# Kernel tuning notes

Hardware: AMD Instinct MI355X
Metric: run time of the kernel (lower is better)

Reference implementation:

```python
import jax, jax.numpy as jnp
import numpy as np
import math

HIDDEN = 8
HEADS = 2
HEAD_DIM = HIDDEN // HEADS  # 4
MAX_SEQ = 102
B, S = 4096, 102


def _rotary_cache(seq_len, head_dim):
    # Matches _create_rotary_embeddings: dim = head_dim//2, inv_freq over arange(0, dim, 2)
    pos = jnp.arange(seq_len, dtype=jnp.float32)
    dim = head_dim // 2
    inv_freq = 1.0 / (10000.0 ** (jnp.arange(0, dim, 2, dtype=jnp.float32) / dim))
    sinusoid = pos[:, None] * inv_freq[None, :]           # [seq, dim//2] -> [102, 1]
    return jnp.stack([jnp.sin(sinusoid), jnp.cos(sinusoid)], axis=0)  # [2, seq, 1]


def _apply_rotary(x, cos, sin):
    # x: [B, H, S, hd]; cos/sin: [2, S, 1] (faithful to the source's buggy unpack,
    # which broadcasts the stacked sin/cos pair across the H==2 head dim)
    x2 = jnp.stack([-x[..., 1::2], x[..., ::2]], axis=-1).reshape(x.shape)
    return x * cos + x2 * sin


def setup_inputs() -> dict:
    key = jax.random.key(0)
    kq, kk, kv, k1, k2, k3, k4 = jax.random.split(key, 7)
    scale = 1.0 / math.sqrt(HIDDEN)
    return {
        "query": jax.random.normal(kq, (B, S, HIDDEN), dtype=jnp.float32),
        "key": jax.random.normal(kk, (B, S, HIDDEN), dtype=jnp.float32),
        "value": jax.random.normal(kv, (B, S, HIDDEN), dtype=jnp.float32),
        "wq": jax.random.normal(k1, (HIDDEN, HIDDEN), dtype=jnp.float32) * scale,
        "wk": jax.random.normal(k2, (HIDDEN, HIDDEN), dtype=jnp.float32) * scale,
        "wv": jax.random.normal(k3, (HIDDEN, HIDDEN), dtype=jnp.float32) * scale,
        "wo": jax.random.normal(k4, (HIDDEN, HIDDEN), dtype=jnp.float32) * scale,
    }


def reference(query, key, value, wq, wk, wv, wo):
    b, sq, _ = query.shape
    sk = key.shape[1]
    # nn.Linear (no bias): y = x @ W^T
    q = query @ wq.T
    k = key @ wk.T
    v = value @ wv.T
    # b n (h d) -> b h n d
    def split_heads(t, s):
        return t.reshape(b, s, HEADS, HEAD_DIM).transpose(0, 2, 1, 3)
    q = split_heads(q, sq)
    k = split_heads(k, sk)
    v = split_heads(v, sk)
    cache = _rotary_cache(MAX_SEQ, HEAD_DIM)
    sin_t = cache[:, :sq]  # [2, sq, 1] (named 'sin' in source, holds stacked sin/cos)
    cos_t = cache[:, :sk]  # [2, sk, 1]
    q = _apply_rotary(q, cos_t, sin_t)
    k = _apply_rotary(k, cos_t, sin_t)
    scale = 1.0 / math.sqrt(HEAD_DIM)
    # chunk_size = min(sk, 1024) = sk -> single chunk == full softmax attention
    scores = jnp.einsum('bhqd,bhkd->bhqk', q, k) * scale  # [B, H, Sq, Sk]
    attn = jax.nn.softmax(scores, axis=-1)
    out = jnp.einsum('bhqk,bhkd->bhqd', attn, v)
    # b h n d -> b n (h d)
    out = out.transpose(0, 2, 1, 3).reshape(b, sq, HIDDEN)
    return out @ wo.T
```

## Files before the change

### kernel.cpp

```cpp
#include <hip/hip_runtime.h>

#define NB 4096
#define SS 102
#define QSCALE 0.72134752044448170368f

typedef float v2f __attribute__((ext_vector_type(2)));
typedef __fp16 h2 __attribute__((ext_vector_type(2)));
typedef __fp16 h8 __attribute__((ext_vector_type(8)));

__global__ __launch_bounds__(256) void mha_fused_kernel(
    const float* __restrict__ query, const float* __restrict__ key,
    const float* __restrict__ value, const float* __restrict__ wq,
    const float* __restrict__ wk, const float* __restrict__ wvp,
    const float* __restrict__ wo, float* __restrict__ out)
{
    __shared__ __align__(16) unsigned char lds[17264];
    float*  RAW  = (float*)lds;
    float*  QF   = (float*)(lds + 9792);
    float*  ROTT = (float*)(lds + 13120);
    __fp16* KV   = (__fp16*)(lds + 13936);
    float*  COMB = (float*)lds;
    float*  PART = (float*)(lds + 3264);

    const int t = threadIdx.x;
    const int b = blockIdx.x;

    float4 rq, rk, rv;
    if (t < 204) {
        const float4* q4 = (const float4*)(query + (size_t)b * 816);
        const float4* k4 = (const float4*)(key   + (size_t)b * 816);
        const float4* v4 = (const float4*)(value + (size_t)b * 816);
        rq = q4[t]; rk = k4[t]; rv = v4[t];
    }

    if (t < SS) {
        const float ang = (float)t;
        ROTT[2 * t]     = sinf(ang);
        ROTT[2 * t + 1] = cosf(ang);
    }
    if (t >= 208 && t < 212) {
        const int z = t - 208;
        *(float4*)(QF + (((z >> 1) * 104) + SS + (z & 1)) * 4) =
            (float4){0.f, 0.f, 0.f, 0.f};
    }

    if (t < 204) {
        float4* R4 = (float4*)RAW;
        R4[t]       = rq;
        R4[204 + t] = rk;
        R4[408 + t] = rv;
    }
    __syncthreads();

    {
        const int wvu  = __builtin_amdgcn_readfirstlane(t >> 6);
        const int lane = t & 63;
        if (wvu < 3) {
            const float* W = (wvu == 0) ? wq : (wvu == 1) ? wk : wvp;
            for (int r = lane; r < SS; r += 64) {
                const float4 a = *(const float4*)(RAW + (wvu * SS + r) * 8);
                const float4 c = *(const float4*)(RAW + (wvu * SS + r) * 8 + 4);
                float x[8];
#pragma unroll
                for (int ch = 0; ch < 8; ++ch) {
                    x[ch] = a.x * W[ch * 8 + 0] + a.y * W[ch * 8 + 1]
                          + a.z * W[ch * 8 + 2] + a.w * W[ch * 8 + 3]
                          + c.x * W[ch * 8 + 4] + c.y * W[ch * 8 + 5]
                          + c.z * W[ch * 8 + 6] + c.w * W[ch * 8 + 7];
                }
                if (wvu == 2) {
#pragma unroll
                    for (int h = 0; h < 2; ++h) {
                        __fp16* rec = KV + (h * 104 + r) * 8;
                        *(h2*)(rec + 4) = __builtin_amdgcn_cvt_pkrtz(x[4*h+0], x[4*h+1]);
                        *(h2*)(rec + 6) = __builtin_amdgcn_cvt_pkrtz(x[4*h+2], x[4*h+3]);
                    }
                } else {
                    const float2 sc = *(const float2*)(ROTT + 2 * r);
#pragma unroll
                    for (int h = 0; h < 2; ++h) {
                        float w = (h == 0) ? sc.x : sc.y;
                        if (wvu == 0) w *= QSCALE;
                        const float y0 = (x[4*h+0] - x[4*h+1]) * w;
                        const float y1 = (x[4*h+1] + x[4*h+0]) * w;
                        const float y2 = (x[4*h+2] - x[4*h+3]) * w;
                        const float y3 = (x[4*h+3] + x[4*h+2]) * w;
                        if (wvu == 0) {
                            *(float4*)(QF + (h * 104 + r) * 4) =
                                (float4){y0, y1, y2, y3};
                        } else {
                            __fp16* rec = KV + (h * 104 + r) * 8;
                            *(h2*)(rec)     = __builtin_amdgcn_cvt_pkrtz(y0, y1);
                            *(h2*)(rec + 2) = __builtin_amdgcn_cvt_pkrtz(y2, y3);
                        }
                    }
                }
            }
        }
    }
    __syncthreads();

    {
        const int wv   = t >> 6, lane = t & 63;
        const int h    = wv >> 1, kh = wv & 1;
        const bool act = lane < 52;
        v2f acc0 = {0.f, 0.f}, acc1 = {0.f, 0.f},
            acc2 = {0.f, 0.f}, acc3 = {0.f, 0.f}, L = {0.f, 0.f};
        if (act) {
            const float4 qa = *(const float4*)(QF + (h * 104 + 2 * lane) * 4);
            const float4 qc = *(const float4*)(QF + (h * 104 + 2 * lane + 1) * 4);
            const v2f q0 = {qa.x, qc.x}, q1 = {qa.y, qc.y},
                      q2 = {qa.z, qc.z}, q3 = {qa.w, qc.w};
            const __fp16* KVh = KV + (h * 104 + kh * 51) * 8;
            for (int j = 0; j < 51; ++j) {
                const h8 rec = *(const h8*)(KVh + j * 8);
                const float k0 = (float)rec[0], k1 = (float)rec[1];
                const float k2 = (float)rec[2], k3 = (float)rec[3];
                const float v0 = (float)rec[4], v1 = (float)rec[5];
                const float v2 = (float)rec[6], v3 = (float)rec[7];
                v2f s = q0 * k0 + q1 * k1 + q2 * k2 + q3 * k3;
                v2f p;
                p.x = __builtin_amdgcn_exp2f(s.x);
                p.y = __builtin_amdgcn_exp2f(s.y);
                L += p;
                acc0 += p * v0; acc1 += p * v1;
                acc2 += p * v2; acc3 += p * v3;
            }
            if (kh == 1) {
                float* P = PART + (h * 52 + lane) * 10;
                *(v2f*)(P + 0) = acc0; *(v2f*)(P + 2) = acc1;
                *(v2f*)(P + 4) = acc2; *(v2f*)(P + 6) = acc3;
                *(v2f*)(P + 8) = L;
            }
        }
        __syncthreads();
        if (act && kh == 0) {
            const float* P = PART + (h * 52 + lane) * 10;
            acc0 += *(const v2f*)(P + 0); acc1 += *(const v2f*)(P + 2);
            acc2 += *(const v2f*)(P + 4); acc3 += *(const v2f*)(P + 6);
            L    += *(const v2f*)(P + 8);
            const float a0[2] = {acc0.x, acc0.y}, a1[2] = {acc1.x, acc1.y};
            const float a2[2] = {acc2.x, acc2.y}, a3[2] = {acc3.x, acc3.y};
            const float ll[2] = {L.x, L.y};
#pragma unroll
            for (int j = 0; j < 2; ++j) {
                const int row = 2 * lane + j;
                if (row < SS) {
                    const float inv = 1.f / ll[j];
                    *(float4*)(COMB + row * 8 + h * 4) =
                        (float4){a0[j] * inv, a1[j] * inv, a2[j] * inv, a3[j] * inv};
                }
            }
        }
    }
    __syncthreads();

    if (t < SS) {
        const float4 a = *(const float4*)(COMB + t * 8);
        const float4 c = *(const float4*)(COMB + t * 8 + 4);
        float x[8];
#pragma unroll
        for (int ch = 0; ch < 8; ++ch) {
            x[ch] = a.x * wo[ch * 8 + 0] + a.y * wo[ch * 8 + 1]
                  + a.z * wo[ch * 8 + 2] + a.w * wo[ch * 8 + 3]
                  + c.x * wo[ch * 8 + 4] + c.y * wo[ch * 8 + 5]
                  + c.z * wo[ch * 8 + 6] + c.w * wo[ch * 8 + 7];
        }
        float* o = out + (size_t)b * 816 + t * 8;
        *(float4*)(o)     = (float4){x[0], x[1], x[2], x[3]};
        *(float4*)(o + 4) = (float4){x[4], x[5], x[6], x[7]};
    }
}

extern "C" void kernel_launch(void* const* d_in, const int* in_sizes, int n_in,
                              void* d_out, int out_size, void* d_ws, size_t ws_size,
                              hipStream_t stream) {
    const float* query = (const float*)d_in[0];
    const float* key   = (const float*)d_in[1];
    const float* value = (const float*)d_in[2];
    const float* wq    = (const float*)d_in[3];
    const float* wk    = (const float*)d_in[4];
    const float* wv    = (const float*)d_in[5];
    const float* wo    = (const float*)d_in[6];
    float* out = (float*)d_out;
    mha_fused_kernel<<<NB, 256, 0, stream>>>(query, key, value, wq, wk, wv, wo, out);
}
```

Measured before the change: 122.7 us.

## Map one batch element per wavefront with fp16 staging and fdot2 scores

Each wavefront now handles a whole batch element, so each 256-thread block covers four elements in private LDS slices and all __syncthreads barriers go away. Raw inputs and Q are staged in fp16, and attention scores use packed fdot2 on half pairs. Each lane now covers four query rows over all 102 keys, which removes the split-key partial combine. sin/cos come from fast intrinsics in registers instead of an LDS table. The costs are lower precision (inputs and Q rounded to fp16, plus approximate sin/cos at angles up to 101) and more registers per lane.

After: 121.4 us. About the same (-1.0%).

```diff
diff --git a/kernel.cpp b/kernel.cpp
--- a/kernel.cpp
+++ b/kernel.cpp
@@ -1,174 +1,162 @@
 #include <hip/hip_runtime.h>
 
-#define NB 4096
 #define SS 102
 #define QSCALE 0.72134752044448170368f
 
-typedef float v2f __attribute__((ext_vector_type(2)));
 typedef __fp16 h2 __attribute__((ext_vector_type(2)));
+typedef __fp16 h4 __attribute__((ext_vector_type(4)));
 typedef __fp16 h8 __attribute__((ext_vector_type(8)));
 
-__global__ __launch_bounds__(256) void mha_fused_kernel(
+__device__ __forceinline__ void store4h(__fp16* p, float a, float b,
+                                        float c, float d) {
+    h2 lo = __builtin_amdgcn_cvt_pkrtz(a, b);
+    h2 hi = __builtin_amdgcn_cvt_pkrtz(c, d);
+    *(h4*)p = __builtin_shufflevector(lo, hi, 0, 1, 2, 3);
+}
+
+__global__ __launch_bounds__(256, 4) void mha_fused_kernel(
     const float* __restrict__ query, const float* __restrict__ key,
     const float* __restrict__ value, const float* __restrict__ wq,
     const float* __restrict__ wk, const float* __restrict__ wvp,
     const float* __restrict__ wo, float* __restrict__ out)
 {
-    __shared__ __align__(16) unsigned char lds[17264];
-    float*  RAW  = (float*)lds;
-    float*  QF   = (float*)(lds + 9792);
-    float*  ROTT = (float*)(lds + 13120);
-    __fp16* KV   = (__fp16*)(lds + 13936);
-    float*  COMB = (float*)lds;
-    float*  PART = (float*)(lds + 3264);
+    __shared__ __align__(16) unsigned char lds[4 * 9792];
+    const int t = threadIdx.x;
+    const int w = t >> 6, lane = t & 63;
+    unsigned char* base = lds + w * 9792;
+    __fp16* RAWH = (__fp16*)base;
+    __fp16* QH   = (__fp16*)(base + 4896);
+    __fp16* KV   = (__fp16*)(base + 6528);
+    float*  COMB = (float*)base;
 
-    const int t = threadIdx.x;
-    const int b = blockIdx.x;
+    const size_t b = (size_t)blockIdx.x * 4 + w;
 
-    float4 rq, rk, rv;
-    if (t < 204) {
-        const float4* q4 = (const float4*)(query + (size_t)b * 816);
-        const float4* k4 = (const float4*)(key   + (size_t)b * 816);
-        const float4* v4 = (const float4*)(value + (size_t)b * 816);
-        rq = q4[t]; rk = k4[t]; rv = v4[t];
+    const float4* q4 = (const float4*)(query + b * 816);
+    const float4* k4 = (const float4*)(key   + b * 816);
+    const float4* v4 = (const float4*)(value + b * 816);
+    float4 rq[4], rk[4], rv[4];
+#pragma unroll
+    for (int c = 0; c < 4; ++c) {
+        const int i = lane + 64 * c;
+        if (i < 204) { rq[c] = q4[i]; rk[c] = k4[i]; rv[c] = v4[i]; }
+    }
+#pragma unroll
+    for (int c = 0; c < 4; ++c) {
+        const int i = lane + 64 * c;
+        if (i < 204) {
+            store4h(RAWH + i * 4,        rq[c].x, rq[c].y, rq[c].z, rq[c].w);
+            store4h(RAWH + 816 + i * 4,  rk[c].x, rk[c].y, rk[c].z, rk[c].w);
+            store4h(RAWH + 1632 + i * 4, rv[c].x, rv[c].y, rv[c].z, rv[c].w);
+        }
     }
 
-    if (t < SS) {
-        const float ang = (float)t;
-        ROTT[2 * t]     = sinf(ang);
-        ROTT[2 * t + 1] = cosf(ang);
+    float snv[2], csv[2];
+#pragma unroll
+    for (int c = 0; c < 2; ++c) {
+        const int r = lane + 64 * c;
+        snv[c] = __sinf((float)r);
+        csv[c] = __cosf((float)r);
     }
-    if (t >= 208 && t < 212) {
-        const int z = t - 208;
-        *(float4*)(QF + (((z >> 1) * 104) + SS + (z & 1)) * 4) =
-            (float4){0.f, 0.f, 0.f, 0.f};
-    }
-
-    if (t < 204) {
-        float4* R4 = (float4*)RAW;
-        R4[t]       = rq;
-        R4[204 + t] = rk;
-        R4[408 + t] = rv;
-    }
-    __syncthreads();
-
-    {
-        const int wvu  = __builtin_amdgcn_readfirstlane(t >> 6);
-        const int lane = t & 63;
-        if (wvu < 3) {
-            const float* W = (wvu == 0) ? wq : (wvu == 1) ? wk : wvp;
-            for (int r = lane; r < SS; r += 64) {
-                const float4 a = *(const float4*)(RAW + (wvu * SS + r) * 8);
-                const float4 c = *(const float4*)(RAW + (wvu * SS + r) * 8 + 4);
+#pragma unroll
+    for (int T = 0; T < 3; ++T) {
+        const float* W = (T == 0) ? wq : (T == 1) ? wk : wvp;
+#pragma unroll
+        for (int c = 0; c < 2; ++c) {
+            const int r = lane + 64 * c;
+            if (r < SS) {
+                const h8 raw = *(const h8*)(RAWH + T * 816 + r * 8);
                 float x[8];
 #pragma unroll
                 for (int ch = 0; ch < 8; ++ch) {
-                    x[ch] = a.x * W[ch * 8 + 0] + a.y * W[ch * 8 + 1]
-                          + a.z * W[ch * 8 + 2] + a.w * W[ch * 8 + 3]
-                          + c.x * W[ch * 8 + 4] + c.y * W[ch * 8 + 5]
-                          + c.z * W[ch * 8 + 6] + c.w * W[ch * 8 + 7];
+                    float acc = 0.f;
+#pragma unroll
+                    for (int j = 0; j < 8; ++j)
+                        acc += (float)raw[j] * W[ch * 8 + j];
+                    x[ch] = acc;
                 }
-                if (wvu == 2) {
+                if (T == 2) {
+                    store4h(KV + (0 * SS + r) * 8 + 4, x[0], x[1], x[2], x[3]);
+                    store4h(KV + (1 * SS + r) * 8 + 4, x[4], x[5], x[6], x[7]);
+                } else {
 #pragma unroll
                     for (int h = 0; h < 2; ++h) {
-                        __fp16* rec = KV + (h * 104 + r) * 8;
-                        *(h2*)(rec + 4) = __builtin_amdgcn_cvt_pkrtz(x[4*h+0], x[4*h+1]);
-                        *(h2*)(rec + 6) = __builtin_amdgcn_cvt_pkrtz(x[4*h+2], x[4*h+3]);
-                    }
-                } else {
-                    const float2 sc = *(const float2*)(ROTT + 2 * r);
-#pragma unroll
-                    for (int h = 0; h < 2; ++h) {
-                        float w = (h == 0) ? sc.x : sc.y;
-                        if (wvu == 0) w *= QSCALE;
-                        const float y0 = (x[4*h+0] - x[4*h+1]) * w;
-                        const float y1 = (x[4*h+1] + x[4*h+0]) * w;
-                        const float y2 = (x[4*h+2] - x[4*h+3]) * w;
-                        const float y3 = (x[4*h+3] + x[4*h+2]) * w;
-                        if (wvu == 0) {
-                            *(float4*)(QF + (h * 104 + r) * 4) =
-                                (float4){y0, y1, y2, y3};
-                        } else {
-                            __fp16* rec = KV + (h * 104 + r) * 8;
-                            *(h2*)(rec)     = __builtin_amdgcn_cvt_pkrtz(y0, y1);
-                            *(h2*)(rec + 2) = __builtin_amdgcn_cvt_pkrtz(y2, y3);
-                        }
+                        float wr = h ? csv[c] : snv[c];
+                        if (T == 0) wr *= QSCALE;
+                        const float y0 = (x[4*h+0] - x[4*h+1]) * wr;
+                        const float y1 = (x[4*h+1] + x[4*h+0]) * wr;
+                        const float y2 = (x[4*h+2] - x[4*h+3]) * wr;
+                        const float y3 = (x[4*h+3] + x[4*h+2]) * wr;
+                        if (T == 0) store4h(QH + (h * SS + r) * 4, y0, y1, y2, y3);
+                        else        store4h(KV + (h * SS + r) * 8, y0, y1, y2, y3);
                     }
                 }
             }
         }
     }
-    __syncthreads();
 
     {
-        const int wv   = t >> 6, lane = t & 63;
-        const int h    = wv >> 1, kh = wv & 1;
-        const bool act = lane < 52;
-        v2f acc0 = {0.f, 0.f}, acc1 = {0.f, 0.f},
-            acc2 = {0.f, 0.f}, acc3 = {0.f, 0.f}, L = {0.f, 0.f};
-        if (act) {
-            const float4 qa = *(const float4*)(QF + (h * 104 + 2 * lane) * 4);
-            const float4 qc = *(const float4*)(QF + (h * 104 + 2 * lane + 1) * 4);
-            const v2f q0 = {qa.x, qc.x}, q1 = {qa.y, qc.y},
-                      q2 = {qa.z, qc.z}, q3 = {qa.w, qc.w};
-            const __fp16* KVh = KV + (h * 104 + kh * 51) * 8;
-            for (int j = 0; j < 51; ++j) {
-                const h8 rec = *(const h8*)(KVh + j * 8);
-                const float k0 = (float)rec[0], k1 = (float)rec[1];
-                const float k2 = (float)rec[2], k3 = (float)rec[3];
-                const float v0 = (float)rec[4], v1 = (float)rec[5];
-                const float v2 = (float)rec[6], v3 = (float)rec[7];
-                v2f s = q0 * k0 + q1 * k1 + q2 * k2 + q3 * k3;
-                v2f p;
-                p.x = __builtin_amdgcn_exp2f(s.x);
-                p.y = __builtin_amdgcn_exp2f(s.y);
-                L += p;
-                acc0 += p * v0; acc1 += p * v1;
-                acc2 += p * v2; acc3 += p * v3;
-            }
-            if (kh == 1) {
-                float* P = PART + (h * 52 + lane) * 10;
-                *(v2f*)(P + 0) = acc0; *(v2f*)(P + 2) = acc1;
-                *(v2f*)(P + 4) = acc2; *(v2f*)(P + 6) = acc3;
-                *(v2f*)(P + 8) = L;
+        const int h   = lane >> 5;
+        const int idx = lane & 31;
+        h2 qlo[4], qhi[4];
+        int rows[4]; bool ract[4];
+#pragma unroll
+        for (int c = 0; c < 4; ++c) {
+            int r = idx + 32 * c;
+            ract[c] = (r < SS);
+            if (!ract[c]) r = 0;
+            rows[c] = r;
+            const h4 q = *(const h4*)(QH + (h * SS + r) * 4);
+            qlo[c] = __builtin_shufflevector(q, q, 0, 1);
+            qhi[c] = __builtin_shufflevector(q, q, 2, 3);
+        }
+        float a0[4] = {}, a1[4] = {}, a2[4] = {}, a3[4] = {}, L[4] = {};
+        const __fp16* KVh = KV + h * SS * 8;
+#pragma unroll 2
+        for (int k = 0; k < SS; ++k) {
+            const h8 rec = *(const h8*)(KVh + k * 8);
+            const h2 k01 = {rec[0], rec[1]};
+            const h2 k23 = {rec[2], rec[3]};
+            const float v0 = (float)rec[4], v1 = (float)rec[5];
+            const float v2 = (float)rec[6], v3 = (float)rec[7];
+#pragma unroll
+            for (int c = 0; c < 4; ++c) {
+                const float s = __builtin_amdgcn_fdot2(
+                    k01, qlo[c],
+                    __builtin_amdgcn_fdot2(k23, qhi[c], 0.f, false), false);
+                const float p = __builtin_amdgcn_exp2f(s);
+                L[c] += p;
+                a0[c] += p * v0; a1[c] += p * v1;
+                a2[c] += p * v2; a3[c] += p * v3;
             }
         }
-        __syncthreads();
-        if (act && kh == 0) {
-            const float* P = PART + (h * 52 + lane) * 10;
-            acc0 += *(const v2f*)(P + 0); acc1 += *(const v2f*)(P + 2);
-            acc2 += *(const v2f*)(P + 4); acc3 += *(const v2f*)(P + 6);
-            L    += *(const v2f*)(P + 8);
-            const float a0[2] = {acc0.x, acc0.y}, a1[2] = {acc1.x, acc1.y};
-            const float a2[2] = {acc2.x, acc2.y}, a3[2] = {acc3.x, acc3.y};
-            const float ll[2] = {L.x, L.y};
 #pragma unroll
-            for (int j = 0; j < 2; ++j) {
-                const int row = 2 * lane + j;
-                if (row < SS) {
-                    const float inv = 1.f / ll[j];
-                    *(float4*)(COMB + row * 8 + h * 4) =
-                        (float4){a0[j] * inv, a1[j] * inv, a2[j] * inv, a3[j] * inv};
-                }
+        for (int c = 0; c < 4; ++c) {
+            if (ract[c]) {
+                const float inv = 1.f / L[c];
+                *(float4*)(COMB + rows[c] * 8 + h * 4) =
+                    (float4){a0[c] * inv, a1[c] * inv, a2[c] * inv, a3[c] * inv};
             }
         }
     }
-    __syncthreads();
 
-    if (t < SS) {
-        const float4 a = *(const float4*)(COMB + t * 8);
-        const float4 c = *(const float4*)(COMB + t * 8 + 4);
-        float x[8];
 #pragma unroll
-        for (int ch = 0; ch < 8; ++ch) {
-            x[ch] = a.x * wo[ch * 8 + 0] + a.y * wo[ch * 8 + 1]
-                  + a.z * wo[ch * 8 + 2] + a.w * wo[ch * 8 + 3]
-                  + c.x * wo[ch * 8 + 4] + c.y * wo[ch * 8 + 5]
-                  + c.z * wo[ch * 8 + 6] + c.w * wo[ch * 8 + 7];
+    for (int c = 0; c < 2; ++c) {
+        const int r = lane + 64 * c;
+        if (r < SS) {
+            const float4 a = *(const float4*)(COMB + r * 8);
+            const float4 d = *(const float4*)(COMB + r * 8 + 4);
+            float x[8];
+#pragma unroll
+            for (int ch = 0; ch < 8; ++ch) {
+                x[ch] = a.x * wo[ch * 8 + 0] + a.y * wo[ch * 8 + 1]
+                      + a.z * wo[ch * 8 + 2] + a.w * wo[ch * 8 + 3]
+                      + d.x * wo[ch * 8 + 4] + d.y * wo[ch * 8 + 5]
+                      + d.z * wo[ch * 8 + 6] + d.w * wo[ch * 8 + 7];
+            }
+            float* o = out + b * 816 + r * 8;
+            *(float4*)(o)     = (float4){x[0], x[1], x[2], x[3]};
+            *(float4*)(o + 4) = (float4){x[4], x[5], x[6], x[7]};
         }
-        float* o = out + (size_t)b * 816 + t * 8;
-        *(float4*)(o)     = (float4){x[0], x[1], x[2], x[3]};
-        *(float4*)(o + 4) = (float4){x[4], x[5], x[6], x[7]};
     }
 }
 
@@ -183,5 +171,5 @@
     const float* wv    = (const float*)d_in[5];
     const float* wo    = (const float*)d_in[6];
     float* out = (float*)d_out;
-    mha_fused_kernel<<<NB, 256, 0, stream>>>(query, key, value, wq, wk, wv, wo, out);
+    mha_fused_kernel<<<1024, 256, 0, stream>>>(query, key, value, wq, wk, wv, wo, out);
 }
```
